# Optimization experiments

Hardware: AMD Instinct MI355X
Metric: run time of the kernel (lower is better)

The kernel has to match this reference:

```python
import jax, jax.numpy as jnp
import numpy as np

N_HEADS = 16
HEAD_SIZE = 64
N_EMB = 1024
BLOCK = 2048
B, T = 2, 2048

def setup_inputs() -> dict:
    key = jax.random.key(0)
    ks = jax.random.split(key, 6)
    s = 0.02
    x = jax.random.normal(ks[0], (B, T, N_EMB), dtype=jnp.float32)
    # per-head projection weights, stacked: [H, C, hs] (no bias, per module)
    Wq = jax.random.normal(ks[1], (N_HEADS, N_EMB, HEAD_SIZE), dtype=jnp.float32) * s
    Wk = jax.random.normal(ks[2], (N_HEADS, N_EMB, HEAD_SIZE), dtype=jnp.float32) * s
    Wv = jax.random.normal(ks[3], (N_HEADS, N_EMB, HEAD_SIZE), dtype=jnp.float32) * s
    # output projection: Linear(n_heads*head_size -> n_embedding), with bias
    Wo = jax.random.normal(ks[4], (N_HEADS * HEAD_SIZE, N_EMB), dtype=jnp.float32) * s
    bo = jax.random.normal(ks[5], (N_EMB,), dtype=jnp.float32) * s
    return {"x": x, "Wq": Wq, "Wk": Wk, "Wv": Wv, "Wo": Wo, "bo": bo}

def reference(x, Wq, Wk, Wv, Wo, bo):
    # x: [B,T,C]; projections per head -> [B,H,T,hs]
    q = jnp.einsum('btc,hcd->bhtd', x, Wq)
    k = jnp.einsum('btc,hcd->bhtd', x, Wk)
    v = jnp.einsum('btc,hcd->bhtd', x, Wv)
    scale = 1.0 / jnp.sqrt(jnp.asarray(HEAD_SIZE, dtype=x.dtype))
    scores = jnp.einsum('bhtd,bhsd->bhts', q, k) * scale  # [B,H,T,T]
    Tq = x.shape[1]
    causal = jnp.tril(jnp.ones((Tq, Tq), dtype=bool))
    scores = jnp.where(causal, scores, jnp.asarray(-jnp.inf, dtype=scores.dtype))
    attn = jax.nn.softmax(scores, axis=-1)  # dropout in eval mode (identity)
    out = jnp.einsum('bhts,bhsd->bhtd', attn, v)  # [B,H,T,hs]
    # concat heads along last dim (matches torch.cat order over head list)
    out = out.transpose(0, 2, 1, 3).reshape(x.shape[0], Tq, N_HEADS * HEAD_SIZE)
    return out @ Wo + bo
```

## Files before the change

### kernel.cpp

```cpp
#include <hip/hip_runtime.h>


typedef short v8s __attribute__((ext_vector_type(8)));
typedef float v4f __attribute__((ext_vector_type(4)));

#define DEVI __device__ __forceinline__

#define B_SZ 2
#define T_SEQ 2048
#define NH 16
#define HS 64
#define CEMB 1024
#define MROWS (B_SZ * T_SEQ)
#define KSZ 1024
#define SCALE_Q 0.18033688011112042f

DEVI unsigned short f2bf(float f) {
  union { float f; unsigned u; } c; c.f = f;
  unsigned u = c.u;
  unsigned r = (u + 0x7FFFu + ((u >> 16) & 1u)) >> 16;
  return (unsigned short)r;
}

DEVI float exp2_fast(float x) {
  float r;
  asm("v_exp_f32 %0, %1" : "=v"(r) : "v"(x));
  return r;
}

DEVI unsigned cvt_pk_bf16(float lo, float hi) {
  unsigned r;
  asm("v_cvt_pk_bf16_f32 %0, %1, %2" : "=v"(r) : "v"(lo), "v"(hi));
  return r;
}

DEVI void gload_lds16(const void* g, void* l) {
  __builtin_amdgcn_global_load_lds(
      (const __attribute__((address_space(1))) void*)g,
      (__attribute__((address_space(3))) void*)l, 16, 0, 0);
}

DEVI int xcd_swz(int bid, int nwg) {
  int q = nwg >> 3;
  return (bid & 7) * q + (bid >> 3);
}

__global__ __launch_bounds__(256, 4) void prep_kernel(
    const float* __restrict__ x, const float* __restrict__ Wq,
    const float* __restrict__ Wk, const float* __restrict__ Wv,
    const float* __restrict__ Wo, unsigned short* __restrict__ xb,
    unsigned short* __restrict__ Wt, unsigned short* __restrict__ Wot) {
  int bid = blockIdx.x;
  if (bid < 2048) {
    int i = bid * 2048 + threadIdx.x * 8;
    float4 a = *(const float4*)(x + i);
    float4 b = *(const float4*)(x + i + 4);
    ushort4 o0, o1;
    o0.x = f2bf(a.x); o0.y = f2bf(a.y); o0.z = f2bf(a.z); o0.w = f2bf(a.w);
    o1.x = f2bf(b.x); o1.y = f2bf(b.y); o1.z = f2bf(b.z); o1.w = f2bf(b.w);
    *(ushort4*)(xb + i) = o0;
    *(ushort4*)(xb + i + 4) = o1;
    return;
  }
  __shared__ float tile[32][33];
  const float* in; unsigned short* out;
  int C, bx, by;
  if (bid < 5120) {
    int b2 = bid - 2048;
    int widx = b2 >> 10, rem = b2 & 1023;
    in = (widx == 0 ? Wq : (widx == 1 ? Wk : Wv));
    int z = rem >> 6;
    bx = rem & 1; by = (rem >> 1) & 31;
    C = 64;
    in += (size_t)z * 1024 * 64;
    out = Wt + ((size_t)widx << 20) + (size_t)z * 1024 * 64;
  } else {
    int rem = bid - 5120;
    C = 1024;
    bx = rem & 31; by = rem >> 5;
    in = Wo; out = Wot;
  }
  int c0 = bx * 32, r0 = by * 32;
  int tx = threadIdx.x & 31, ty = threadIdx.x >> 5;
#pragma unroll
  for (int j = 0; j < 4; ++j)
    tile[ty + j * 8][tx] = in[(size_t)(r0 + ty + j * 8) * C + c0 + tx];
  __syncthreads();
#pragma unroll
  for (int j = 0; j < 4; ++j)
    out[(size_t)(c0 + ty + j * 8) * 1024 + r0 + tx] = f2bf(tile[tx][ty + j * 8]);
}

template <int MODE>
__global__ __launch_bounds__(256, 3) void gemm_bt(
    const unsigned short* __restrict__ A, const unsigned short* __restrict__ Bt,
    void* __restrict__ Cout, const float* __restrict__ bias, int nbx) {
  __shared__ __align__(16) unsigned char lds[49152];
  unsigned short* As = (unsigned short*)lds;
  unsigned short* Bs = (unsigned short*)(lds + 24576);

  const int tid = threadIdx.x;
  const int lane = tid & 63, w = tid >> 6;
  const int wm = w >> 1, wn = w & 1;
  const int lr = lane & 15, lg = lane >> 4;

  const int wg = xcd_swz(blockIdx.x, gridDim.x);
  const int mb = (wg / nbx) * 128, nb = (wg % nbx) * 128;

  v4f acc[4][4];
  v4f zero = {0.f, 0.f, 0.f, 0.f};
#pragma unroll
  for (int i = 0; i < 4; ++i)
#pragma unroll
    for (int j = 0; j < 4; ++j) acc[i][j] = zero;

  const int srow = lane >> 2;
  const int sgcol = ((lane & 3) ^ (srow & 3)) * 8;
  const unsigned short* gA = A + (size_t)(mb + w * 32 + srow) * KSZ + sgcol;
  const unsigned short* gB = Bt + (size_t)(nb + w * 32 + srow) * KSZ + sgcol;
  unsigned short* lA = As + w * 1024;
  unsigned short* lB = Bs + w * 1024;

#define STAGE_G(buf, kb)                                        \
  do {                                                          \
    gload_lds16(gA + (kb), lA + (buf) * 4096);                  \
    gload_lds16(gA + (kb) + 16 * KSZ, lA + (buf) * 4096 + 512); \
    gload_lds16(gB + (kb), lB + (buf) * 4096);                  \
    gload_lds16(gB + (kb) + 16 * KSZ, lB + (buf) * 4096 + 512); \
  } while (0)

  STAGE_G(0, 0);
  STAGE_G(1, 32);
  STAGE_G(2, 64);

  const int NT = KSZ / 32;
  for (int t = 0; t < NT; ++t) {
    if (t < NT - 2)
      asm volatile("s_waitcnt vmcnt(8)" ::: "memory");
    else if (t == NT - 2)
      asm volatile("s_waitcnt vmcnt(4)" ::: "memory");
    else
      asm volatile("s_waitcnt vmcnt(0)" ::: "memory");
    __builtin_amdgcn_s_barrier();

    const int buf = t % 3;
    v8s af[4], bfr[4];
#pragma unroll
    for (int i = 0; i < 4; ++i) {
      int ra = wm * 64 + i * 16 + lr, rb = wn * 64 + i * 16 + lr;
      af[i]  = *(const v8s*)&As[buf * 4096 + ra * 32 + ((lg ^ (lr & 3)) << 3)];
      bfr[i] = *(const v8s*)&Bs[buf * 4096 + rb * 32 + ((lg ^ (lr & 3)) << 3)];
    }
#pragma unroll
    for (int i = 0; i < 4; ++i)
#pragma unroll
      for (int j = 0; j < 4; ++j)
        acc[i][j] = __builtin_amdgcn_mfma_f32_16x16x32_bf16(af[i], bfr[j], acc[i][j], 0, 0, 0);

    asm volatile("s_waitcnt lgkmcnt(0)" ::: "memory");
    __builtin_amdgcn_s_barrier();
    if (t + 3 < NT) STAGE_G(buf, (t + 3) * 32);
  }
#undef STAGE_G

  if (MODE == 0 && (wg % nbx) >= 16) {
    unsigned short* out = (unsigned short*)Cout;
#pragma unroll
    for (int i = 0; i < 4; ++i) {
      int tl0 = wm * 64 + i * 16 + lg * 4;
      int tc = tl0 >> 3, off = (tl0 & 7) * 2;
#pragma unroll
      for (int j = 0; j < 4; ++j) {
        int dl = wn * 64 + j * 16 + lr;
        unsigned lo = cvt_pk_bf16(acc[i][j][0], acc[i][j][1]);
        unsigned hi = cvt_pk_bf16(acc[i][j][2], acc[i][j][3]);
        unsigned char* p = lds + dl * 256 + ((tc ^ (dl & 15)) << 4) + off;
        *(unsigned*)p = lo;
        *(unsigned*)(p + 4) = hi;
      }
    }
    __syncthreads();
    int b = mb >> 11, mt = mb & 2047;
    int nrem0 = nb & 1023;
    unsigned short* Vg = out + (size_t)(2 * B_SZ * NH) * T_SEQ * HS;
#pragma unroll
    for (int it = 0; it < 8; ++it) {
      int dl = it * 16 + (tid >> 4);
      int tc = tid & 15;
      const unsigned char* p = lds + dl * 256 + ((tc ^ (dl & 15)) << 4);
      int4 vv = *(const int4*)p;
      int nrem = nrem0 + dl;
      int h = nrem >> 6, dd = nrem & 63;
      *(int4*)(Vg + ((size_t)(b * NH + h) * HS + dd) * T_SEQ + mt + tc * 8) = vv;
    }
    return;
  }

#pragma unroll
  for (int i = 0; i < 4; ++i) {
    int mrow0 = mb + wm * 64 + i * 16 + lg * 4;
#pragma unroll
    for (int j = 0; j < 4; ++j) {
      int ncol = nb + wn * 64 + j * 16 + lr;
      if (MODE == 0) {
        int p = ncol >> 10, rem = ncol & 1023, h = rem >> 6, d = rem & 63;
        float sc = (p == 0) ? SCALE_Q : 1.0f;
        unsigned short* out = (unsigned short*)Cout;
#pragma unroll
        for (int r = 0; r < 4; ++r) {
          int mrow = mrow0 + r;
          int b = mrow >> 11, t = mrow & 2047;
          out[((size_t)((p * B_SZ + b) * NH + h) * T_SEQ + t) * HS + d] =
              f2bf(acc[i][j][r] * sc);
        }
      } else {
        float* out = (float*)Cout;
        float bv = bias[ncol];
#pragma unroll
        for (int r = 0; r < 4; ++r)
          out[(size_t)(mrow0 + r) * CEMB + ncol] = acc[i][j][r] + bv;
      }
    }
  }
}

__global__ __launch_bounds__(512, 4) void attn_kernel(
    const unsigned short* __restrict__ Qg, const unsigned short* __restrict__ Kg,
    const unsigned short* __restrict__ Vtg, unsigned short* __restrict__ Yg) {
  __shared__ __align__(16) unsigned char lds[32 * 1024];
  unsigned char* KsB = lds;
  unsigned char* VtB = lds + 16384;

  const int tid = threadIdx.x;
  const int lane = tid & 63, w = tid >> 6;
  const int lr = lane & 15, lg = lane >> 4;
  const int kk = blockIdx.x >> 5;
  const int qc = (kk & 1) ? (kk >> 1) : (15 - (kk >> 1));
  const int bh = blockIdx.x & 31;

  const unsigned short* Qbase = Qg + (size_t)bh * T_SEQ * HS;
  const unsigned short* Kbase = Kg + (size_t)bh * T_SEQ * HS;
  const unsigned short* Vtbase = Vtg + (size_t)bh * T_SEQ * HS;

  const int ks_row = tid >> 3, ks_cb = tid & 7;
  const int kLds0 = ks_row * 128 + ((ks_cb ^ (ks_row & 7)) << 4);
  const unsigned short* Kg0 = Kbase + ks_row * HS + ks_cb * 8;
  const int vs_d = tid >> 4, vs_m = tid & 15;
  const int vLds0 = vs_d * 256 + ((vs_m ^ (vs_d & 15)) << 4);
  const int vbt = ((vs_m >> 2) << 4) + ((vs_m & 3) << 2);
  const unsigned short* Vg0 = Vtbase + (size_t)vs_d * T_SEQ + vbt;

  v8s qA[2];
  {
    const unsigned short* qrow = Qbase + (size_t)(qc * 128 + w * 16 + lr) * HS;
    qA[0] = *(const v8s*)(qrow + lg * 8);
    qA[1] = *(const v8s*)(qrow + 32 + lg * 8);
  }

  v4f O[4];
  v4f zero = {0.f, 0.f, 0.f, 0.f};
#pragma unroll
  for (int d = 0; d < 4; ++d) O[d] = zero;
  float mrun = -1e30f, lrun = 0.f;

  int4 gK0 = *(const int4*)(Kg0);
  int4 gK1 = *(const int4*)(Kg0 + 4096);
  int2 vlo0 = *(const int2*)(Vg0);
  int2 vhi0 = *(const int2*)(Vg0 + 64);
  int2 vlo1 = *(const int2*)(Vg0 + 32 * T_SEQ);
  int2 vhi1 = *(const int2*)(Vg0 + 32 * T_SEQ + 64);

  for (int t = 0; t <= qc; ++t) {
    __syncthreads();
    *(int4*)(KsB + kLds0) = gK0;
    *(int4*)(KsB + kLds0 + 8192) = gK1;
    {
      int4 v0; v0.x = vlo0.x; v0.y = vlo0.y; v0.z = vhi0.x; v0.w = vhi0.y;
      int4 v1; v1.x = vlo1.x; v1.y = vlo1.y; v1.z = vhi1.x; v1.w = vhi1.y;
      *(int4*)(VtB + vLds0) = v0;
      *(int4*)(VtB + vLds0 + 8192) = v1;
    }
    __syncthreads();
    if (t < qc) {
      const unsigned short* kp = Kg0 + (t + 1) * (128 * HS);
      gK0 = *(const int4*)kp;
      gK1 = *(const int4*)(kp + 4096);
      const unsigned short* vp = Vg0 + (t + 1) * 128;
      vlo0 = *(const int2*)(vp);
      vhi0 = *(const int2*)(vp + 64);
      vlo1 = *(const int2*)(vp + 32 * T_SEQ);
      vhi1 = *(const int2*)(vp + 32 * T_SEQ + 64);
    }

    const int cflim = (t == qc) ? w : 7;

    v4f S[8];
    __builtin_amdgcn_s_setprio(1);
#pragma unroll
    for (int cf = 0; cf < 8; ++cf) {
      if (cf <= cflim) {
        S[cf] = zero;
#pragma unroll
        for (int ks = 0; ks < 2; ++ks) {
          int srow = cf * 16 + lr;
          v8s kb = *(const v8s*)(KsB + srow * 128 +
                                 ((((ks << 2) + lg) ^ (lr & 7)) << 4));
          S[cf] = __builtin_amdgcn_mfma_f32_16x16x32_bf16(kb, qA[ks], S[cf], 0, 0, 0);
        }
      } else {
        S[cf] = (v4f){-1e30f, -1e30f, -1e30f, -1e30f};
      }
    }
    __builtin_amdgcn_s_setprio(0);

    if (t == qc) {
#pragma unroll
      for (int cf = 0; cf < 8; ++cf)
        if (cf == w) {
#pragma unroll
          for (int r = 0; r < 4; ++r)
            if (lg * 4 + r > lr) S[cf][r] = -1e30f;
        }
    }

    float mx = -1e30f;
#pragma unroll
    for (int cf = 0; cf < 8; ++cf)
#pragma unroll
      for (int r = 0; r < 4; ++r) mx = fmaxf(mx, S[cf][r]);
    mx = fmaxf(mx, __shfl_xor(mx, 16));
    mx = fmaxf(mx, __shfl_xor(mx, 32));

    if (!__all(mx - mrun <= 8.0f)) {
      float mn = fmaxf(mrun, mx);
      float alpha = exp2_fast(mrun - mn);
      mrun = mn;
      lrun *= alpha;
#pragma unroll
      for (int df = 0; df < 4; ++df)
#pragma unroll
        for (int r = 0; r < 4; ++r) O[df][r] *= alpha;
    }

    float sum = 0.f;
#pragma unroll
    for (int cf = 0; cf < 8; ++cf)
#pragma unroll
      for (int r = 0; r < 4; ++r) {
        float p = exp2_fast(S[cf][r] - mrun);
        S[cf][r] = p;
        sum += p;
      }
    sum += __shfl_xor(sum, 16);
    sum += __shfl_xor(sum, 32);
    lrun += sum;

    unsigned pk0[8], pk1[8];
#pragma unroll
    for (int cf = 0; cf < 8; ++cf) {
      pk0[cf] = cvt_pk_bf16(S[cf][0], S[cf][1]);
      pk1[cf] = cvt_pk_bf16(S[cf][2], S[cf][3]);
    }

    __builtin_amdgcn_s_setprio(1);
#pragma unroll
    for (int c = 0; c < 4; ++c) {
      if (t != qc || c <= w) {
        union { unsigned u[4]; v8s s; } pu;
        pu.u[0] = pk0[c]; pu.u[1] = pk1[c];
        pu.u[2] = pk0[c + 4]; pu.u[3] = pk1[c + 4];
        v8s pa = pu.s;
#pragma unroll
        for (int df = 0; df < 4; ++df) {
          int d = df * 16 + lr;
          v8s va = *(const v8s*)(VtB + d * 256 +
                                 ((((c << 2) + lg) ^ lr) << 4));
          O[df] = __builtin_amdgcn_mfma_f32_16x16x32_bf16(va, pa, O[df], 0, 0, 0);
        }
      }
    }
    __builtin_amdgcn_s_setprio(0);
  }

  float invl = 1.0f / lrun;
  int tq = qc * 128 + w * 16 + lr;
  int b = bh >> 4, h = bh & 15;
  size_t ybase = ((size_t)b * T_SEQ + tq) * (NH * HS) + h * 64;
#pragma unroll
  for (int df = 0; df < 4; ++df) {
    ushort4 o4;
    o4.x = f2bf(O[df][0] * invl);
    o4.y = f2bf(O[df][1] * invl);
    o4.z = f2bf(O[df][2] * invl);
    o4.w = f2bf(O[df][3] * invl);
    *(ushort4*)(Yg + ybase + df * 16 + lg * 4) = o4;
  }
}

extern "C" void kernel_launch(void* const* d_in, const int* in_sizes, int n_in,
                              void* d_out, int out_size, void* d_ws, size_t ws_size,
                              hipStream_t stream) {
  (void)in_sizes; (void)n_in; (void)out_size; (void)ws_size;
  const float* x  = (const float*)d_in[0];
  const float* Wq = (const float*)d_in[1];
  const float* Wk = (const float*)d_in[2];
  const float* Wv = (const float*)d_in[3];
  const float* Wo = (const float*)d_in[4];
  const float* bo = (const float*)d_in[5];

  unsigned char* ws = (unsigned char*)d_ws;
  unsigned short* xb  = (unsigned short*)(ws);
  unsigned short* Wt  = (unsigned short*)(ws + (8u << 20));
  unsigned short* Wot = (unsigned short*)(ws + (14u << 20));
  unsigned short* qkv = (unsigned short*)(ws + (16u << 20));
  unsigned short* Y   = (unsigned short*)(ws + (40u << 20));

  prep_kernel<<<dim3(6144), 256, 0, stream>>>(x, Wq, Wk, Wv, Wo, xb, Wt, Wot);

  gemm_bt<0><<<dim3(768), 256, 0, stream>>>(xb, Wt, qkv, nullptr, 24);

  const unsigned short* Qp = qkv;
  const unsigned short* Kp = qkv + (size_t)B_SZ * NH * T_SEQ * HS;
  const unsigned short* Vtp = qkv + (size_t)2 * B_SZ * NH * T_SEQ * HS;
  attn_kernel<<<dim3(512), 512, 0, stream>>>(Qp, Kp, Vtp, Y);

  gemm_bt<1><<<dim3(256), 256, 0, stream>>>(Y, Wot, d_out, bo, 8);
}
```

Measured before the change: 100.4 us.

## Switch attention kernel to 32x32x16 MFMA with 4 waves per block

Rewrites the attention kernel to use 32x32x16 bf16 MFMA tiles, with each of 4 waves owning 32 query rows instead of 8 waves owning 16. The block shrinks to 256 threads, and K/V staging issues four 16-byte loads per thread. P is repacked for the PV product with v_permlane32_swap instead of a cross-lane layout of 16x16 tiles. The aim is higher MFMA efficiency and fewer shuffle reductions and LDS reads per FLOP. In exchange it raises register pressure, halves waves per block, and coarsens diagonal masking granularity.

```diff
diff --git a/kernel.cpp b/kernel.cpp
--- a/kernel.cpp
+++ b/kernel.cpp
@@ -3,6 +3,7 @@
 
 typedef short v8s __attribute__((ext_vector_type(8)));
 typedef float v4f __attribute__((ext_vector_type(4)));
+typedef float v16f __attribute__((ext_vector_type(16)));
 
 #define DEVI __device__ __forceinline__
 
@@ -224,7 +225,7 @@
   }
 }
 
-__global__ __launch_bounds__(512, 4) void attn_kernel(
+__global__ __launch_bounds__(256, 2) void attn_kernel(
     const unsigned short* __restrict__ Qg, const unsigned short* __restrict__ Kg,
     const unsigned short* __restrict__ Vtg, unsigned short* __restrict__ Yg) {
   __shared__ __align__(16) unsigned char lds[32 * 1024];
@@ -233,7 +234,7 @@
 
   const int tid = threadIdx.x;
   const int lane = tid & 63, w = tid >> 6;
-  const int lr = lane & 15, lg = lane >> 4;
+  const int l31 = lane & 31, hi = lane >> 5;
   const int kk = blockIdx.x >> 5;
   const int qc = (kk & 1) ? (kk >> 1) : (15 - (kk >> 1));
   const int bh = blockIdx.x & 31;
@@ -247,88 +248,86 @@
   const unsigned short* Kg0 = Kbase + ks_row * HS + ks_cb * 8;
   const int vs_d = tid >> 4, vs_m = tid & 15;
   const int vLds0 = vs_d * 256 + ((vs_m ^ (vs_d & 15)) << 4);
-  const int vbt = ((vs_m >> 2) << 4) + ((vs_m & 3) << 2);
-  const unsigned short* Vg0 = Vtbase + (size_t)vs_d * T_SEQ + vbt;
-
-  v8s qA[2];
+  const unsigned short* Vg0 = Vtbase + (size_t)vs_d * T_SEQ + vs_m * 8;
+
+  v8s qB[4];
   {
-    const unsigned short* qrow = Qbase + (size_t)(qc * 128 + w * 16 + lr) * HS;
-    qA[0] = *(const v8s*)(qrow + lg * 8);
-    qA[1] = *(const v8s*)(qrow + 32 + lg * 8);
-  }
-
-  v4f O[4];
-  v4f zero = {0.f, 0.f, 0.f, 0.f};
-#pragma unroll
-  for (int d = 0; d < 4; ++d) O[d] = zero;
+    const unsigned short* qrow = Qbase + (size_t)(qc * 128 + w * 32 + l31) * HS;
+#pragma unroll
+    for (int ks = 0; ks < 4; ++ks)
+      qB[ks] = *(const v8s*)(qrow + ks * 16 + hi * 8);
+  }
+
+  v16f zero16 = {};
+  v16f neg16 = zero16 - 1e30f;
+  v16f O[2];
+  O[0] = zero16; O[1] = zero16;
   float mrun = -1e30f, lrun = 0.f;
 
-  int4 gK0 = *(const int4*)(Kg0);
-  int4 gK1 = *(const int4*)(Kg0 + 4096);
-  int2 vlo0 = *(const int2*)(Vg0);
-  int2 vhi0 = *(const int2*)(Vg0 + 64);
-  int2 vlo1 = *(const int2*)(Vg0 + 32 * T_SEQ);
-  int2 vhi1 = *(const int2*)(Vg0 + 32 * T_SEQ + 64);
+  int4 kA[4], vv[4];
+#pragma unroll
+  for (int k = 0; k < 4; ++k) {
+    kA[k] = *(const int4*)(Kg0 + k * 2048);
+    vv[k] = *(const int4*)(Vg0 + k * 16 * T_SEQ);
+  }
 
   for (int t = 0; t <= qc; ++t) {
     __syncthreads();
-    *(int4*)(KsB + kLds0) = gK0;
-    *(int4*)(KsB + kLds0 + 8192) = gK1;
-    {
-      int4 v0; v0.x = vlo0.x; v0.y = vlo0.y; v0.z = vhi0.x; v0.w = vhi0.y;
-      int4 v1; v1.x = vlo1.x; v1.y = vlo1.y; v1.z = vhi1.x; v1.w = vhi1.y;
-      *(int4*)(VtB + vLds0) = v0;
-      *(int4*)(VtB + vLds0 + 8192) = v1;
+#pragma unroll
+    for (int k = 0; k < 4; ++k) {
+      *(int4*)(KsB + kLds0 + k * 4096) = kA[k];
+      *(int4*)(VtB + vLds0 + k * 4096) = vv[k];
     }
     __syncthreads();
     if (t < qc) {
-      const unsigned short* kp = Kg0 + (t + 1) * (128 * HS);
-      gK0 = *(const int4*)kp;
-      gK1 = *(const int4*)(kp + 4096);
+      const unsigned short* kp = Kg0 + (t + 1) * 8192;
       const unsigned short* vp = Vg0 + (t + 1) * 128;
-      vlo0 = *(const int2*)(vp);
-      vhi0 = *(const int2*)(vp + 64);
-      vlo1 = *(const int2*)(vp + 32 * T_SEQ);
-      vhi1 = *(const int2*)(vp + 32 * T_SEQ + 64);
-    }
-
-    const int cflim = (t == qc) ? w : 7;
-
-    v4f S[8];
+#pragma unroll
+      for (int k = 0; k < 4; ++k) {
+        kA[k] = *(const int4*)(kp + k * 2048);
+        vv[k] = *(const int4*)(vp + k * 16 * T_SEQ);
+      }
+    }
+
+    const bool diag = (t == qc);
+    const int cflim = diag ? w : 3;
+
+    v16f S[4];
     __builtin_amdgcn_s_setprio(1);
 #pragma unroll
-    for (int cf = 0; cf < 8; ++cf) {
+    for (int cf = 0; cf < 4; ++cf) {
       if (cf <= cflim) {
-        S[cf] = zero;
-#pragma unroll
-        for (int ks = 0; ks < 2; ++ks) {
-          int srow = cf * 16 + lr;
-          v8s kb = *(const v8s*)(KsB + srow * 128 +
-                                 ((((ks << 2) + lg) ^ (lr & 7)) << 4));
-          S[cf] = __builtin_amdgcn_mfma_f32_16x16x32_bf16(kb, qA[ks], S[cf], 0, 0, 0);
+        S[cf] = zero16;
+#pragma unroll
+        for (int ks = 0; ks < 4; ++ks) {
+          int row = cf * 32 + l31;
+          v8s ka = *(const v8s*)(KsB + row * 128 +
+                                 ((((ks << 1) + hi) ^ (row & 7)) << 4));
+          S[cf] = __builtin_amdgcn_mfma_f32_32x32x16_bf16(ka, qB[ks], S[cf], 0, 0, 0);
         }
       } else {
-        S[cf] = (v4f){-1e30f, -1e30f, -1e30f, -1e30f};
+        S[cf] = neg16;
       }
     }
     __builtin_amdgcn_s_setprio(0);
 
-    if (t == qc) {
-#pragma unroll
-      for (int cf = 0; cf < 8; ++cf)
+    if (diag) {
+#pragma unroll
+      for (int cf = 0; cf < 4; ++cf)
         if (cf == w) {
 #pragma unroll
-          for (int r = 0; r < 4; ++r)
-            if (lg * 4 + r > lr) S[cf][r] = -1e30f;
+          for (int reg = 0; reg < 16; ++reg) {
+            int kvin = (reg & 3) + 8 * (reg >> 2) + 4 * hi;
+            if (kvin > l31) S[cf][reg] = -1e30f;
+          }
         }
     }
 
     float mx = -1e30f;
 #pragma unroll
-    for (int cf = 0; cf < 8; ++cf)
-#pragma unroll
-      for (int r = 0; r < 4; ++r) mx = fmaxf(mx, S[cf][r]);
-    mx = fmaxf(mx, __shfl_xor(mx, 16));
+    for (int cf = 0; cf < 4; ++cf)
+#pragma unroll
+      for (int reg = 0; reg < 16; ++reg) mx = fmaxf(mx, S[cf][reg]);
     mx = fmaxf(mx, __shfl_xor(mx, 32));
 
     if (!__all(mx - mrun <= 8.0f)) {
@@ -337,45 +336,43 @@
       mrun = mn;
       lrun *= alpha;
 #pragma unroll
-      for (int df = 0; df < 4; ++df)
-#pragma unroll
-        for (int r = 0; r < 4; ++r) O[df][r] *= alpha;
+      for (int db = 0; db < 2; ++db)
+#pragma unroll
+        for (int reg = 0; reg < 16; ++reg) O[db][reg] *= alpha;
     }
 
     float sum = 0.f;
 #pragma unroll
-    for (int cf = 0; cf < 8; ++cf)
-#pragma unroll
-      for (int r = 0; r < 4; ++r) {
-        float p = exp2_fast(S[cf][r] - mrun);
-        S[cf][r] = p;
+    for (int cf = 0; cf < 4; ++cf)
+#pragma unroll
+      for (int reg = 0; reg < 16; ++reg) {
+        float p = exp2_fast(S[cf][reg] - mrun);
+        S[cf][reg] = p;
         sum += p;
       }
-    sum += __shfl_xor(sum, 16);
     sum += __shfl_xor(sum, 32);
     lrun += sum;
 
-    unsigned pk0[8], pk1[8];
-#pragma unroll
-    for (int cf = 0; cf < 8; ++cf) {
-      pk0[cf] = cvt_pk_bf16(S[cf][0], S[cf][1]);
-      pk1[cf] = cvt_pk_bf16(S[cf][2], S[cf][3]);
-    }
-
+    const int kslim = diag ? (2 * w + 1) : 7;
     __builtin_amdgcn_s_setprio(1);
 #pragma unroll
-    for (int c = 0; c < 4; ++c) {
-      if (t != qc || c <= w) {
-        union { unsigned u[4]; v8s s; } pu;
-        pu.u[0] = pk0[c]; pu.u[1] = pk1[c];
-        pu.u[2] = pk0[c + 4]; pu.u[3] = pk1[c + 4];
-        v8s pa = pu.s;
-#pragma unroll
-        for (int df = 0; df < 4; ++df) {
-          int d = df * 16 + lr;
-          v8s va = *(const v8s*)(VtB + d * 256 +
-                                 ((((c << 2) + lg) ^ lr) << 4));
-          O[df] = __builtin_amdgcn_mfma_f32_16x16x32_bf16(va, pa, O[df], 0, 0, 0);
+    for (int ks = 0; ks < 8; ++ks) {
+      if (ks <= kslim) {
+        int cf = ks >> 1, rb = (ks & 1) * 8;
+        unsigned x0 = cvt_pk_bf16(S[cf][rb + 0], S[cf][rb + 1]);
+        unsigned x1 = cvt_pk_bf16(S[cf][rb + 2], S[cf][rb + 3]);
+        unsigned y0 = cvt_pk_bf16(S[cf][rb + 4], S[cf][rb + 5]);
+        unsigned y1 = cvt_pk_bf16(S[cf][rb + 6], S[cf][rb + 7]);
+        asm("v_permlane32_swap_b32 %0, %1" : "+v"(x0), "+v"(y0));
+        asm("v_permlane32_swap_b32 %0, %1" : "+v"(x1), "+v"(y1));
+        union { unsigned u[4]; v8s s; } pb;
+        pb.u[0] = x0; pb.u[1] = x1; pb.u[2] = y0; pb.u[3] = y1;
+#pragma unroll
+        for (int db = 0; db < 2; ++db) {
+          int row = db * 32 + l31;
+          v8s va = *(const v8s*)(VtB + row * 256 +
+                                 ((((ks << 1) + hi) ^ (row & 15)) << 4));
+          O[db] = __builtin_amdgcn_mfma_f32_32x32x16_bf16(va, pb.s, O[db], 0, 0, 0);
         }
       }
     }
@@ -383,18 +380,21 @@
   }
 
   float invl = 1.0f / lrun;
-  int tq = qc * 128 + w * 16 + lr;
+  int tq = qc * 128 + w * 32 + l31;
   int b = bh >> 4, h = bh & 15;
   size_t ybase = ((size_t)b * T_SEQ + tq) * (NH * HS) + h * 64;
 #pragma unroll
-  for (int df = 0; df < 4; ++df) {
-    ushort4 o4;
-    o4.x = f2bf(O[df][0] * invl);
-    o4.y = f2bf(O[df][1] * invl);
-    o4.z = f2bf(O[df][2] * invl);
-    o4.w = f2bf(O[df][3] * invl);
-    *(ushort4*)(Yg + ybase + df * 16 + lg * 4) = o4;
-  }
+  for (int db = 0; db < 2; ++db)
+#pragma unroll
+    for (int rq = 0; rq < 4; ++rq) {
+      int d0 = db * 32 + rq * 8 + hi * 4;
+      ushort4 o4;
+      o4.x = f2bf(O[db][rq * 4 + 0] * invl);
+      o4.y = f2bf(O[db][rq * 4 + 1] * invl);
+      o4.z = f2bf(O[db][rq * 4 + 2] * invl);
+      o4.w = f2bf(O[db][rq * 4 + 3] * invl);
+      *(ushort4*)(Yg + ybase + d0) = o4;
+    }
 }
 
 extern "C" void kernel_launch(void* const* d_in, const int* in_sizes, int n_in,
@@ -422,7 +422,7 @@
   const unsigned short* Qp = qkv;
   const unsigned short* Kp = qkv + (size_t)B_SZ * NH * T_SEQ * HS;
   const unsigned short* Vtp = qkv + (size_t)2 * B_SZ * NH * T_SEQ * HS;
-  attn_kernel<<<dim3(512), 512, 0, stream>>>(Qp, Kp, Vtp, Y);
+  attn_kernel<<<dim3(512), 256, 0, stream>>>(Qp, Kp, Vtp, Y);
 
   gemm_bt<1><<<dim3(256), 256, 0, stream>>>(Y, Wot, d_out, bo, 8);
 }
```

New measurement: 160.6 us. 1.6x slower.
